# Performance work log

Hardware: AMD Instinct MI355X
Metric: run time of the kernel (lower is better)

## Reference

```python
import jax, jax.numpy as jnp
import numpy as np

B, S, D_IN, D_OUT = 8, 4096, 1024, 1024
R_F, R_M, R_S = 8, 32, 64
R_TOT = R_F + R_M + R_S  # 104
HID = 64
ALPHA = 1.0


def setup_inputs() -> dict:
    key = jax.random.key(0)
    ks = jax.random.split(key, 10)
    inp = {
        "x": jax.random.normal(ks[0], (B, S, D_IN), dtype=jnp.float32),
        # fresh memory state after reset_memory(): zeros of shape [batch, r_*]
        "mem_fast": jnp.zeros((B, R_F), dtype=jnp.float32),
        "mem_medium": jnp.zeros((B, R_M), dtype=jnp.float32),
        "mem_slow": jnp.zeros((B, R_S), dtype=jnp.float32),
        # frozen base nn.Linear
        "base_w": jax.random.normal(ks[1], (D_OUT, D_IN), dtype=jnp.float32) / np.sqrt(D_IN),
        "base_b": jax.random.normal(ks[2], (D_OUT,), dtype=jnp.float32) * 0.01,
        # LoRA projections: proj_down kaiming-ish, proj_up zero-init per _init_weights
        "pd_w": jax.random.normal(ks[3], (R_TOT, D_IN), dtype=jnp.float32) / np.sqrt(D_IN),
        "pu_w": jax.random.normal(ks[4], (D_OUT, R_TOT), dtype=jnp.float32) * 0.01,
        # gate_net: Linear(D_IN, HID) -> GELU -> Linear(HID, 3) -> Softmax
        "g1_w": jax.random.normal(ks[5], (HID, D_IN), dtype=jnp.float32) / np.sqrt(D_IN),
        "g1_b": jnp.zeros((HID,), dtype=jnp.float32),
        "g2_w": jax.random.normal(ks[6], (3, HID), dtype=jnp.float32) / np.sqrt(HID),
        "g2_b": jnp.zeros((3,), dtype=jnp.float32),
    }
    return inp


def reference(x, mem_fast, mem_medium, mem_slow, base_w, base_b,
              pd_w, pu_w, g1_w, g1_b, g2_w, g2_b):
    # base linear: [B,S,D_out]
    base_out = jnp.einsum("bsd,od->bso", x, base_w) + base_b
    # down projection: [B,S,R_TOT]
    proj = jnp.einsum("bsd,rd->bsr", x, pd_w)
    # per-timescale multiplicative modulation by recurrent memory state
    # (split -> (1+mem)*proj -> concat) == concat memories once
    mem = jnp.concatenate([mem_fast, mem_medium, mem_slow], axis=-1)  # [B,R_TOT]
    modulated = proj * (1.0 + mem[:, None, :])
    # gate_net: Linear -> GELU(exact) -> Linear -> softmax over 3 timescales
    h = jax.nn.gelu(jnp.einsum("bsd,hd->bsh", x, g1_w) + g1_b, approximate=False)
    gates = jax.nn.softmax(jnp.einsum("bsh,gh->bsg", h, g2_w) + g2_b, axis=-1)
    gate_scale = jnp.mean(gates, axis=-1, keepdims=True)  # [B,S,1]
    # up projection and residual combine
    lora_out = jnp.einsum("bsr,or->bso", modulated, pu_w)
    output = base_out + ALPHA * lora_out * gate_scale
    return output
```

## Files before the change

kernel.cpp:

```cpp
#include <hip/hip_runtime.h>
#include <stdint.h>


typedef unsigned short ushort_t;
typedef unsigned short us8 __attribute__((ext_vector_type(8)));
typedef short short8 __attribute__((ext_vector_type(8)));
typedef float f32x4 __attribute__((ext_vector_type(4)));

__device__ __forceinline__ ushort_t f2b(float f) {
  union { float f; uint32_t i; } v; v.f = f;
  uint32_t lsb = (v.i >> 16) & 1u;
  v.i += 0x7fffu + lsb;
  return (ushort_t)(v.i >> 16);
}

__device__ __forceinline__ void async16(const void* g, void* l) {
  __builtin_amdgcn_global_load_lds(
      (const __attribute__((address_space(1))) void*)g,
      (__attribute__((address_space(3))) void*)l, 16, 0, 0);
}

__global__ __launch_bounds__(256) void convert_x(const float* __restrict__ x,
                                                 ushort_t* __restrict__ xb) {
  const int flat = blockIdx.x;
  const int b = flat & 7;
  const int c = flat >> 3;
  const size_t i = (((size_t)b * 2048 + c) * 256 + threadIdx.x) * 8;
  f32x4 a0 = *(const f32x4*)(x + i);
  f32x4 a1 = *(const f32x4*)(x + i + 4);
  us8 o;
#pragma unroll
  for (int j = 0; j < 4; j++) { o[j] = f2b(a0[j]); o[4 + j] = f2b(a1[j]); }
  *(us8*)(xb + i) = o;
}

__global__ __launch_bounds__(128) void prep(const float* __restrict__ base_w,
                                            const float* __restrict__ pu_w,
                                            const float* __restrict__ pd_w,
                                            const float* __restrict__ mf,
                                            const float* __restrict__ mm,
                                            const float* __restrict__ ms,
                                            ushort_t* __restrict__ W0,
                                            ushort_t* __restrict__ Weff,
                                            int* __restrict__ flags) {
  const int o = blockIdx.x, y = blockIdx.y, t = threadIdx.x;
  __shared__ float spu[104];
  __shared__ int sflag;
  ushort_t* dst;

  if (y == 0) {
    if (t < 104) spu[t] = pu_w[o * 104 + t] * (1.0f / 3.0f);
    dst = W0 + o * 1024;
    __syncthreads();
  } else {
    const int b = y - 1;
    if (t == 0) sflag = 0;
    __syncthreads();
    float mv = 0.0f;
    if (t < 104) {
      mv = (t < 8) ? mf[b * 8 + t]
         : (t < 40) ? mm[b * 32 + (t - 8)]
                    : ms[b * 64 + (t - 40)];
      if (mv != 0.0f) sflag = 1;
      spu[t] = pu_w[o * 104 + t] * (1.0f + mv) * (1.0f / 3.0f);
    }
    __syncthreads();
    if (o == 0 && t == 0) flags[b] = sflag;
    if (!sflag) return;
    dst = Weff + ((size_t)b << 20) + o * 1024;
  }

  const int d0 = t * 8;
  float acc[8];
  f32x4 b0 = *(const f32x4*)(base_w + o * 1024 + d0);
  f32x4 b1 = *(const f32x4*)(base_w + o * 1024 + d0 + 4);
#pragma unroll
  for (int j = 0; j < 4; j++) { acc[j] = b0[j]; acc[4 + j] = b1[j]; }
  for (int r = 0; r < 104; r++) {
    f32x4 p0 = *(const f32x4*)(pd_w + r * 1024 + d0);
    f32x4 p1 = *(const f32x4*)(pd_w + r * 1024 + d0 + 4);
    float s = spu[r];
#pragma unroll
    for (int j = 0; j < 4; j++) { acc[j] += s * p0[j]; acc[4 + j] += s * p1[j]; }
  }
  us8 ov;
#pragma unroll
  for (int j = 0; j < 8; j++) ov[j] = f2b(acc[j]);
  *(us8*)(dst + d0) = ov;
}

__global__ __launch_bounds__(256) void gemm_bt(const ushort_t* __restrict__ xb,
                                               const float* __restrict__ base_b,
                                               const ushort_t* __restrict__ W0,
                                               const ushort_t* __restrict__ Weff,
                                               const int* __restrict__ flags,
                                               float* __restrict__ out) {
  const int flat = blockIdx.x;
  const int b  = flat & 7;
  const int i  = flat >> 3;
  const int g  = i >> 6;
  const int r  = i & 63;
  const int bn = r >> 3;
  const int bm = g * 8 + (r & 7);

  const ushort_t* W = flags[b] ? (Weff + ((size_t)b << 20)) : W0;

  __shared__ __align__(16) short As[128 * 32];
  __shared__ __align__(16) short Bs[128 * 32];

  const int t = threadIdx.x;
  const int wave = t >> 6, lane = t & 63;
  const int row16 = lane & 15, quad = lane >> 4;
  const int wm = (wave >> 1) * 64, wn = (wave & 1) * 64;

  const ushort_t* gA = xb + (((size_t)b * 4096 + bm * 128 + (t >> 2)) << 10) + (t & 3) * 8;
  const ushort_t* gB = W + (((size_t)(bn * 128 + (t >> 2))) << 10) + (t & 3) * 8;
  char* lA = (char*)As + wave * 1024;
  char* lB = (char*)Bs + wave * 1024;

  f32x4 acc[4][4] = {};

  for (int k0 = 0; k0 < 1024; k0 += 32) {
    async16(gA + k0, lA);
    async16(gA + k0 + (64 << 10), lA + 4096);
    async16(gB + k0, lB);
    async16(gB + k0 + (64 << 10), lB + 4096);
    __syncthreads();

    short8 af[4], bf[4];
#pragma unroll
    for (int mi = 0; mi < 4; mi++)
      af[mi] = *(const short8*)(As + (wm + mi * 16 + row16) * 32 + quad * 8);
#pragma unroll
    for (int ni = 0; ni < 4; ni++)
      bf[ni] = *(const short8*)(Bs + (wn + ni * 16 + row16) * 32 + quad * 8);
#pragma unroll
    for (int mi = 0; mi < 4; mi++)
#pragma unroll
      for (int ni = 0; ni < 4; ni++)
        acc[mi][ni] = __builtin_amdgcn_mfma_f32_16x16x32_bf16(af[mi], bf[ni],
                                                              acc[mi][ni], 0, 0, 0);
    __syncthreads();
  }

#pragma unroll
  for (int ni = 0; ni < 4; ni++) {
    const int col = bn * 128 + wn + ni * 16 + row16;
    const float bb = base_b[col];
#pragma unroll
    for (int mi = 0; mi < 4; mi++) {
      const int row = bm * 128 + wm + mi * 16 + quad * 4;
#pragma unroll
      for (int i2 = 0; i2 < 4; i2++) {
        out[(((size_t)b * 4096 + row + i2) << 10) + col] = acc[mi][ni][i2] + bb;
      }
    }
  }
}

extern "C" void kernel_launch(void* const* d_in, const int* in_sizes, int n_in,
                              void* d_out, int out_size, void* d_ws, size_t ws_size,
                              hipStream_t stream) {
  const float* x  = (const float*)d_in[0];
  const float* mf = (const float*)d_in[1];
  const float* mm = (const float*)d_in[2];
  const float* ms = (const float*)d_in[3];
  const float* base_w = (const float*)d_in[4];
  const float* base_b = (const float*)d_in[5];
  const float* pd_w = (const float*)d_in[6];
  const float* pu_w = (const float*)d_in[7];

  char* ws = (char*)d_ws;
  int* flags     = (int*)ws;
  ushort_t* W0   = (ushort_t*)(ws + 4096);
  ushort_t* xb   = (ushort_t*)(ws + 4096 + (2u << 20));
  ushort_t* Weff = (ushort_t*)(ws + 4096 + (2u << 20) + (64u << 20));

  prep<<<dim3(1024, 9), 128, 0, stream>>>(base_w, pu_w, pd_w, mf, mm, ms,
                                          W0, Weff, flags);
  convert_x<<<16384, 256, 0, stream>>>(x, xb);
  gemm_bt<<<2048, 256, 0, stream>>>(xb, base_b, W0, Weff, flags, (float*)d_out);
}
```

Before: 349.7 us.

## Replace GEMM with 256x256-tile, 8-wave, 4-stage pipelined LDS kernel

Replaces the 128x128-tile GEMM with a 256x256-tile kernel using 8 waves and 512 threads. It keeps a 4-buffer LDS ring with loads issued two k-steps ahead, and XOR-swizzles the LDS layout to avoid bank conflicts. MFMA work is split into two halves interleaved with async loads, using s_setprio and barriers. This aims to raise data reuse and hide global-load latency. The cost is 128KB of LDS per block, heavy register use, and only 512 blocks, which may underfill 256 CUs or hurt occupancy.

```diff
diff --git a/kernel.cpp b/kernel.cpp
--- a/kernel.cpp
+++ b/kernel.cpp
@@ -89,73 +89,112 @@
   *(us8*)(dst + d0) = ov;
 }
 
-__global__ __launch_bounds__(256) void gemm_bt(const ushort_t* __restrict__ xb,
-                                               const float* __restrict__ base_b,
-                                               const ushort_t* __restrict__ W0,
-                                               const ushort_t* __restrict__ Weff,
-                                               const int* __restrict__ flags,
-                                               float* __restrict__ out) {
+__global__ __launch_bounds__(512, 2) void gemm256(
+    const ushort_t* __restrict__ xb, const float* __restrict__ base_b,
+    const ushort_t* __restrict__ W0, const ushort_t* __restrict__ Weff,
+    const int* __restrict__ flags, float* __restrict__ out) {
   const int flat = blockIdx.x;
   const int b  = flat & 7;
   const int i  = flat >> 3;
-  const int g  = i >> 6;
-  const int r  = i & 63;
-  const int bn = r >> 3;
-  const int bm = g * 8 + (r & 7);
+  const int bm = i >> 2;
+  const int bn = i & 3;
 
   const ushort_t* W = flags[b] ? (Weff + ((size_t)b << 20)) : W0;
 
-  __shared__ __align__(16) short As[128 * 32];
-  __shared__ __align__(16) short Bs[128 * 32];
+  __shared__ __align__(16) char lds[4 * 32768];
 
   const int t = threadIdx.x;
-  const int wave = t >> 6, lane = t & 63;
-  const int row16 = lane & 15, quad = lane >> 4;
-  const int wm = (wave >> 1) * 64, wn = (wave & 1) * 64;
-
-  const ushort_t* gA = xb + (((size_t)b * 4096 + bm * 128 + (t >> 2)) << 10) + (t & 3) * 8;
-  const ushort_t* gB = W + (((size_t)(bn * 128 + (t >> 2))) << 10) + (t & 3) * 8;
-  char* lA = (char*)As + wave * 1024;
-  char* lB = (char*)Bs + wave * 1024;
-
-  f32x4 acc[4][4] = {};
-
-  for (int k0 = 0; k0 < 1024; k0 += 32) {
-    async16(gA + k0, lA);
-    async16(gA + k0 + (64 << 10), lA + 4096);
-    async16(gB + k0, lB);
-    async16(gB + k0 + (64 << 10), lB + 4096);
-    __syncthreads();
-
-    short8 af[4], bf[4];
-#pragma unroll
-    for (int mi = 0; mi < 4; mi++)
-      af[mi] = *(const short8*)(As + (wm + mi * 16 + row16) * 32 + quad * 8);
-#pragma unroll
-    for (int ni = 0; ni < 4; ni++)
-      bf[ni] = *(const short8*)(Bs + (wn + ni * 16 + row16) * 32 + quad * 8);
-#pragma unroll
-    for (int mi = 0; mi < 4; mi++)
-#pragma unroll
-      for (int ni = 0; ni < 4; ni++)
-        acc[mi][ni] = __builtin_amdgcn_mfma_f32_16x16x32_bf16(af[mi], bf[ni],
-                                                              acc[mi][ni], 0, 0, 0);
-    __syncthreads();
-  }
-
-#pragma unroll
-  for (int ni = 0; ni < 4; ni++) {
-    const int col = bn * 128 + wn + ni * 16 + row16;
+  const int w = t >> 6, l = t & 63;
+  const int wr = w >> 2, wc = w & 3;
+  const int row16 = l & 15, quad = l >> 4;
+
+  const int srow = w * 16 + (l >> 2);
+  const int scol = (((l & 3) ^ ((l >> 3) & 3))) * 8;
+  const ushort_t* gA = xb + (((size_t)b * 4096 + bm * 256 + srow) << 10) + scol;
+  const ushort_t* gB = W + (((size_t)(bn * 256 + srow)) << 10) + scol;
+
+  const int qsw = (quad ^ ((row16 >> 1) & 3)) * 16;
+  const int aoff = (wr * 128 + row16) * 64 + qsw;
+  const int boff = 16384 + (wc * 64 + row16) * 64 + qsw;
+
+#define STAGE_A(kt)                                                       \
+  {                                                                       \
+    const int bi_ = (kt) & 3;                                             \
+    const ushort_t* g_ = gA + (kt) * 32;                                  \
+    char* d_ = lds + bi_ * 32768 + w * 1024;                              \
+    async16(g_, d_);                                                      \
+    async16(g_ + (128 << 10), d_ + 8192);                                 \
+  }
+#define STAGE_B(kt)                                                       \
+  {                                                                       \
+    const int bi_ = (kt) & 3;                                             \
+    const ushort_t* g_ = gB + (kt) * 32;                                  \
+    char* d_ = lds + bi_ * 32768 + 16384 + w * 1024;                      \
+    async16(g_, d_);                                                      \
+    async16(g_ + (128 << 10), d_ + 8192);                                 \
+  }
+
+  f32x4 acc[8][4] = {};
+
+  STAGE_A(0) STAGE_B(0) STAGE_A(1) STAGE_B(1)
+  asm volatile("s_waitcnt vmcnt(4)" ::: "memory");
+  __builtin_amdgcn_s_barrier();
+
+  for (int kt = 0; kt < 32; ++kt) {
+    const char* base = lds + (kt & 3) * 32768;
+
+    short8 af[8];
+#pragma unroll
+    for (int mi = 0; mi < 8; ++mi)
+      af[mi] = *(const short8*)(base + aoff + mi * 1024);
+    short8 bf0 = *(const short8*)(base + boff);
+    short8 bf1 = *(const short8*)(base + boff + 1024);
+    if (kt < 30) STAGE_A(kt + 2)
+    __builtin_amdgcn_s_barrier();
+    __builtin_amdgcn_s_setprio(1);
+#pragma unroll
+    for (int mi = 0; mi < 8; ++mi) {
+      acc[mi][0] = __builtin_amdgcn_mfma_f32_16x16x32_bf16(af[mi], bf0, acc[mi][0], 0, 0, 0);
+      acc[mi][1] = __builtin_amdgcn_mfma_f32_16x16x32_bf16(af[mi], bf1, acc[mi][1], 0, 0, 0);
+    }
+    __builtin_amdgcn_s_setprio(0);
+    __builtin_amdgcn_s_barrier();
+
+    short8 bf2 = *(const short8*)(base + boff + 2048);
+    short8 bf3 = *(const short8*)(base + boff + 3072);
+    if (kt < 30) STAGE_B(kt + 2)
+    __builtin_amdgcn_s_barrier();
+    __builtin_amdgcn_s_setprio(1);
+#pragma unroll
+    for (int mi = 0; mi < 8; ++mi) {
+      acc[mi][2] = __builtin_amdgcn_mfma_f32_16x16x32_bf16(af[mi], bf2, acc[mi][2], 0, 0, 0);
+      acc[mi][3] = __builtin_amdgcn_mfma_f32_16x16x32_bf16(af[mi], bf3, acc[mi][3], 0, 0, 0);
+    }
+    __builtin_amdgcn_s_setprio(0);
+
+    if (kt < 30) {
+      asm volatile("s_waitcnt vmcnt(4)" ::: "memory");
+    } else if (kt == 30) {
+      asm volatile("s_waitcnt vmcnt(0)" ::: "memory");
+    }
+    __builtin_amdgcn_s_barrier();
+  }
+
+#pragma unroll
+  for (int ni = 0; ni < 4; ++ni) {
+    const int col = bn * 256 + wc * 64 + ni * 16 + row16;
     const float bb = base_b[col];
 #pragma unroll
-    for (int mi = 0; mi < 4; mi++) {
-      const int row = bm * 128 + wm + mi * 16 + quad * 4;
-#pragma unroll
-      for (int i2 = 0; i2 < 4; i2++) {
-        out[(((size_t)b * 4096 + row + i2) << 10) + col] = acc[mi][ni][i2] + bb;
-      }
-    }
-  }
+    for (int mi = 0; mi < 8; ++mi) {
+      const int row = bm * 256 + wr * 128 + mi * 16 + quad * 4;
+      float* po = out + (((size_t)b * 4096 + row) << 10) + col;
+#pragma unroll
+      for (int i2 = 0; i2 < 4; ++i2)
+        po[(size_t)i2 << 10] = acc[mi][ni][i2] + bb;
+    }
+  }
+#undef STAGE_A
+#undef STAGE_B
 }
 
 extern "C" void kernel_launch(void* const* d_in, const int* in_sizes, int n_in,
@@ -179,5 +218,5 @@
   prep<<<dim3(1024, 9), 128, 0, stream>>>(base_w, pu_w, pd_w, mf, mm, ms,
                                           W0, Weff, flags);
   convert_x<<<16384, 256, 0, stream>>>(x, xb);
-  gemm_bt<<<2048, 256, 0, stream>>>(xb, base_b, W0, Weff, flags, (float*)d_out);
-}
+  gemm256<<<512, 512, 0, stream>>>(xb, base_b, W0, Weff, flags, (float*)d_out);
+}
```

New measurement: 347.7 us. About the same (-0.6%).
